# Kernel tuning notes

Measured on AMD Instinct MI355X. Metric: run time of the kernel, lower is better.

The kernel has to match this reference:

```python
import jax, jax.numpy as jnp
import numpy as np

H = 4        # num_heads
R = 5        # dilation_rate
W = 49       # window_size
D = 256      # d_model // 2
B = 32
N = 4900     # must be divisible by W*R = 245


def setup_inputs() -> dict:
    key = jax.random.key(0)
    k1, k2, k3, k4, k5 = jax.random.split(key, 5)
    s = 1.0 / np.sqrt(D)
    return {
        "emb": jax.random.normal(k1, (B, N, D), dtype=jnp.float32),
        "Wq": jax.random.normal(k2, (D, D), dtype=jnp.float32) * s,
        "bq": jax.random.normal(k3, (D,), dtype=jnp.float32) * s,
        "Wo": jax.random.normal(k4, (D, D), dtype=jnp.float32) * s,
        "bo": jax.random.normal(k5, (D,), dtype=jnp.float32) * s,
    }


def reference(emb, Wq, bq, Wo, bo):
    b, n, d = emb.shape
    dh = d // H
    g = n // (W * R)  # number of segments
    # Original forward uses q_proj for q, k AND v (faithful to source bug).
    q = emb @ Wq.T + bq  # [B, N, D]
    # Dilated local windows: token index = g*(W*R) + i*R + r.
    # Tokens sharing (segment g, dilation offset r) attend densely over i in [0, W).
    x = q.reshape(b, g, W, R, H, dh)
    scale = jnp.asarray(dh, q.dtype) ** -0.5
    scores = jnp.einsum("bgirhd,bgjrhd->bgrhij", x, x) * scale  # [B,G,R,H,W,W]
    attn = jax.nn.softmax(scores, axis=-1)
    out = jnp.einsum("bgrhij,bgjrhd->bgirhd", attn, x)  # [B,G,W,R,H,dh]
    out = out.reshape(b, n, d)
    return out @ Wo.T + bo
```

## Files before the change

kernel.cpp:

```cpp
#include <hip/hip_runtime.h>
#include <hip/hip_bf16.h>
#include <math.h>

#define NH     4
#define RD     5
#define WW     49
#define DM     256
#define BATCH  32
#define NTOK   4900
#define GSEG   20
#define SEG    245

typedef short bf16x8 __attribute__((ext_vector_type(8)));
typedef short bf16x4 __attribute__((ext_vector_type(4)));
typedef float f32x4  __attribute__((ext_vector_type(4)));

__device__ __forceinline__ short f2bf(float f) {
    union { __hip_bfloat16 h; short s; } u;
    u.h = __float2bfloat16(f);
    return u.s;
}

__device__ __forceinline__ int qix(int row, int col) {
    return row * 256 + (col ^ ((row & 7) << 3));
}
__device__ __forceinline__ int tix(int d, int j) {
    return 64 * 256 + d * 64 + (j ^ ((d & 7) << 3));
}

__global__ __launch_bounds__(256)
void wcvt(const float* __restrict__ Wq, const float* __restrict__ Wo,
          short* __restrict__ Wqb, short* __restrict__ Wob) {
    int t = blockIdx.x * 256 + threadIdx.x;
    const float* src = (t < 16384) ? Wq : Wo;
    short* dst = (t < 16384) ? Wqb : Wob;
    int i = (t & 16383) * 4;
    float4 v = *(const float4*)(src + i);
    bf16x4 o = { f2bf(v.x), f2bf(v.y), f2bf(v.z), f2bf(v.w) };
    *(bf16x4*)(dst + i) = o;
}

__global__ __launch_bounds__(256, 2)
void fused(const float* __restrict__ emb, const short* __restrict__ Wqb,
           const float* __restrict__ bq, const short* __restrict__ Wob,
           const float* __restrict__ bo, float* __restrict__ out) {
    __shared__ __align__(16) short sm[64 * 256 + 256 * 64];

    const int tid = threadIdx.x;
    const int wv = tid >> 6, ln = tid & 63, lc = ln & 15, lq = ln >> 4;

    const int bid = blockIdx.x;
    const int L = (bid & 7) * 400 + (bid >> 3);
    const int b = L / 100;
    const int rem = L - b * 100;
    const int g = rem / 5, r = rem - (rem / 5) * 5;
    const size_t tok0 = (size_t)b * NTOK + (size_t)g * SEG + r;
    const int n0 = wv * 64;

    {
        const float* ar[4];
        const short* br[4];
        #pragma unroll
        for (int mi = 0; mi < 4; mi++) {
            int t = mi * 16 + lc;
            t = (t > WW - 1) ? (WW - 1) : t;
            ar[mi] = emb + (tok0 + (size_t)t * RD) * DM + lq * 8;
        }
        #pragma unroll
        for (int ni = 0; ni < 4; ni++)
            br[ni] = Wqb + (size_t)(n0 + ni * 16 + lc) * DM + lq * 8;

        f32x4 acc[4][4] = {};
        for (int k0 = 0; k0 < DM; k0 += 32) {
            bf16x8 af[4], bfr[4];
            #pragma unroll
            for (int mi = 0; mi < 4; mi++) {
                float4 v0 = *(const float4*)(ar[mi] + k0);
                float4 v1 = *(const float4*)(ar[mi] + k0 + 4);
                bf16x8 t8 = { f2bf(v0.x), f2bf(v0.y), f2bf(v0.z), f2bf(v0.w),
                              f2bf(v1.x), f2bf(v1.y), f2bf(v1.z), f2bf(v1.w) };
                af[mi] = t8;
            }
            #pragma unroll
            for (int ni = 0; ni < 4; ni++) bfr[ni] = *(const bf16x8*)(br[ni] + k0);
            #pragma unroll
            for (int mi = 0; mi < 4; mi++)
                #pragma unroll
                for (int ni = 0; ni < 4; ni++)
                    acc[mi][ni] = __builtin_amdgcn_mfma_f32_16x16x32_bf16(
                        af[mi], bfr[ni], acc[mi][ni], 0, 0, 0);
        }
        float bv[4];
        #pragma unroll
        for (int ni = 0; ni < 4; ni++) bv[ni] = bq[n0 + ni * 16 + lc];
        #pragma unroll
        for (int mi = 0; mi < 4; mi++)
            #pragma unroll
            for (int rg = 0; rg < 4; rg++) {
                const int t = mi * 16 + lq * 4 + rg;
                #pragma unroll
                for (int ni = 0; ni < 4; ni++) {
                    const int col = n0 + ni * 16 + lc;
                    const short s = (t < WW) ? f2bf(acc[mi][ni][rg] + bv[ni])
                                             : (short)0;
                    sm[qix(t, col)] = s;
                    sm[tix(col, t)] = s;
                }
            }
    }
    __syncthreads();

    {
        const int c0 = n0;
        bf16x8 xa[4][2];
        #pragma unroll
        for (int mi = 0; mi < 4; mi++) {
            xa[mi][0] = *(const bf16x8*)&sm[qix(mi * 16 + lc, c0 + lq * 8)];
            xa[mi][1] = *(const bf16x8*)&sm[qix(mi * 16 + lc, c0 + 32 + lq * 8)];
        }
        f32x4 sa[4][4] = {};
        #pragma unroll
        for (int mi = 0; mi < 4; mi++)
            #pragma unroll
            for (int ni = 0; ni < 4; ni++) {
                sa[mi][ni] = __builtin_amdgcn_mfma_f32_16x16x32_bf16(
                    xa[mi][0], xa[ni][0], sa[mi][ni], 0, 0, 0);
                sa[mi][ni] = __builtin_amdgcn_mfma_f32_16x16x32_bf16(
                    xa[mi][1], xa[ni][1], sa[mi][ni], 0, 0, 0);
            }
        #pragma unroll
        for (int mi = 0; mi < 4; mi++)
            #pragma unroll
            for (int rg = 0; rg < 4; rg++) {
                float s[4];
                float m = -1e30f;
                #pragma unroll
                for (int ni = 0; ni < 4; ni++) {
                    s[ni] = sa[mi][ni][rg] * 0.125f;
                    if (ni * 16 + lc < WW) m = fmaxf(m, s[ni]);
                }
                m = fmaxf(m, __shfl_xor(m, 1));
                m = fmaxf(m, __shfl_xor(m, 2));
                m = fmaxf(m, __shfl_xor(m, 4));
                m = fmaxf(m, __shfl_xor(m, 8));
                float e4[4], l_ = 0.f;
                #pragma unroll
                for (int ni = 0; ni < 4; ni++) {
                    e4[ni] = (ni * 16 + lc < WW) ? __expf(s[ni] - m) : 0.f;
                    l_ += e4[ni];
                }
                l_ += __shfl_xor(l_, 1);
                l_ += __shfl_xor(l_, 2);
                l_ += __shfl_xor(l_, 4);
                l_ += __shfl_xor(l_, 8);
                const float inv = 1.f / l_;
                const int i = mi * 16 + lq * 4 + rg;
                #pragma unroll
                for (int ni = 0; ni < 4; ni++)
                    sm[qix(i, c0 + ni * 16 + lc)] = f2bf(e4[ni] * inv);
            }
        bf16x8 pa[4][2], pb[4][2];
        #pragma unroll
        for (int mi = 0; mi < 4; mi++) {
            pa[mi][0] = *(const bf16x8*)&sm[qix(mi * 16 + lc, c0 + lq * 8)];
            pa[mi][1] = *(const bf16x8*)&sm[qix(mi * 16 + lc, c0 + 32 + lq * 8)];
        }
        #pragma unroll
        for (int ni = 0; ni < 4; ni++) {
            pb[ni][0] = *(const bf16x8*)&sm[tix(c0 + ni * 16 + lc, lq * 8)];
            pb[ni][1] = *(const bf16x8*)&sm[tix(c0 + ni * 16 + lc, 32 + lq * 8)];
        }
        f32x4 oa[4][4] = {};
        #pragma unroll
        for (int mi = 0; mi < 4; mi++)
            #pragma unroll
            for (int ni = 0; ni < 4; ni++) {
                oa[mi][ni] = __builtin_amdgcn_mfma_f32_16x16x32_bf16(
                    pa[mi][0], pb[ni][0], oa[mi][ni], 0, 0, 0);
                oa[mi][ni] = __builtin_amdgcn_mfma_f32_16x16x32_bf16(
                    pa[mi][1], pb[ni][1], oa[mi][ni], 0, 0, 0);
            }
        #pragma unroll
        for (int mi = 0; mi < 4; mi++)
            #pragma unroll
            for (int rg = 0; rg < 4; rg++) {
                const int i = mi * 16 + lq * 4 + rg;
                if (i < WW) {
                    #pragma unroll
                    for (int ni = 0; ni < 4; ni++)
                        sm[qix(i, c0 + ni * 16 + lc)] = f2bf(oa[mi][ni][rg]);
                }
            }
    }
    __syncthreads();

    {
        const short* br[4];
        #pragma unroll
        for (int ni = 0; ni < 4; ni++)
            br[ni] = Wob + (size_t)(n0 + ni * 16 + lc) * DM + lq * 8;
        int trow[4];
        #pragma unroll
        for (int mi = 0; mi < 4; mi++) {
            int t = mi * 16 + lc;
            trow[mi] = (t > WW - 1) ? (WW - 1) : t;
        }
        f32x4 acc[4][4] = {};
        for (int k0 = 0; k0 < DM; k0 += 32) {
            bf16x8 af[4], bfr[4];
            #pragma unroll
            for (int mi = 0; mi < 4; mi++)
                af[mi] = *(const bf16x8*)&sm[qix(trow[mi], k0 + lq * 8)];
            #pragma unroll
            for (int ni = 0; ni < 4; ni++) bfr[ni] = *(const bf16x8*)(br[ni] + k0);
            #pragma unroll
            for (int mi = 0; mi < 4; mi++)
                #pragma unroll
                for (int ni = 0; ni < 4; ni++)
                    acc[mi][ni] = __builtin_amdgcn_mfma_f32_16x16x32_bf16(
                        af[mi], bfr[ni], acc[mi][ni], 0, 0, 0);
        }
        float bv[4];
        #pragma unroll
        for (int ni = 0; ni < 4; ni++) bv[ni] = bo[n0 + ni * 16 + lc];
        #pragma unroll
        for (int mi = 0; mi < 4; mi++)
            #pragma unroll
            for (int rg = 0; rg < 4; rg++) {
                const int t = mi * 16 + lq * 4 + rg;
                if (t < WW) {
                    float* op = out + (tok0 + (size_t)t * RD) * DM + n0;
                    #pragma unroll
                    for (int ni = 0; ni < 4; ni++)
                        op[ni * 16 + lc] = acc[mi][ni][rg] + bv[ni];
                }
            }
    }
}

extern "C" void kernel_launch(void* const* d_in, const int* in_sizes, int n_in,
                              void* d_out, int out_size, void* d_ws, size_t ws_size,
                              hipStream_t stream) {
    const float* emb = (const float*)d_in[0];
    const float* Wq  = (const float*)d_in[1];
    const float* bq  = (const float*)d_in[2];
    const float* Wo  = (const float*)d_in[3];
    const float* bo  = (const float*)d_in[4];
    float* out = (float*)d_out;

    short* Wqb = (short*)d_ws;
    short* Wob = Wqb + DM * DM;

    wcvt<<<dim3(128), dim3(256), 0, stream>>>(Wq, Wo, Wqb, Wob);
    fused<<<dim3(BATCH * GSEG * RD), dim3(256), 0, stream>>>(
        emb, Wqb, bq, Wob, bo, out);
}
```

Baseline: 473.1 us.

## Split window rows across 8 waves and software-pipeline global loads in GEMMs

Blocks grow from 256 to 512 threads: each of 8 waves now owns 32 token rows by 64 columns instead of 64 rows, which halves accumulator registers per wave and lets launch bounds ask for 4 blocks per CU. The Q and output projection loops are fully unrolled with register double-buffering, so the next k-slice of emb and weights loads while the current MFMAs run. The block-index swizzle across XCDs is removed. An extra barrier separates the score reads from the in-place probability writes, because waves now share rows. The risks are more barriers, duplicate loads of the B-side Q tiles, and possible register spills under the tighter bounds.

```diff
diff --git a/kernel.cpp b/kernel.cpp
--- a/kernel.cpp
+++ b/kernel.cpp
@@ -40,7 +40,7 @@
     *(bf16x4*)(dst + i) = o;
 }
 
-__global__ __launch_bounds__(256, 2)
+__global__ __launch_bounds__(512, 4)
 void fused(const float* __restrict__ emb, const short* __restrict__ Wqb,
            const float* __restrict__ bq, const short* __restrict__ Wob,
            const float* __restrict__ bo, float* __restrict__ out) {
@@ -50,57 +50,87 @@
     const int wv = tid >> 6, ln = tid & 63, lc = ln & 15, lq = ln >> 4;
 
     const int bid = blockIdx.x;
-    const int L = (bid & 7) * 400 + (bid >> 3);
-    const int b = L / 100;
-    const int rem = L - b * 100;
+    const int b = bid / 100;
+    const int rem = bid - b * 100;
     const int g = rem / 5, r = rem - (rem / 5) * 5;
     const size_t tok0 = (size_t)b * NTOK + (size_t)g * SEG + r;
-    const int n0 = wv * 64;
+
+    const int wn = (wv & 3) * 64;
+    const int wm = (wv >> 2) * 32;
 
     {
-        const float* ar[4];
+        const float* ar[2];
         const short* br[4];
         #pragma unroll
-        for (int mi = 0; mi < 4; mi++) {
-            int t = mi * 16 + lc;
+        for (int mi = 0; mi < 2; mi++) {
+            int t = wm + mi * 16 + lc;
             t = (t > WW - 1) ? (WW - 1) : t;
             ar[mi] = emb + (tok0 + (size_t)t * RD) * DM + lq * 8;
         }
         #pragma unroll
         for (int ni = 0; ni < 4; ni++)
-            br[ni] = Wqb + (size_t)(n0 + ni * 16 + lc) * DM + lq * 8;
-
-        f32x4 acc[4][4] = {};
-        for (int k0 = 0; k0 < DM; k0 += 32) {
-            bf16x8 af[4], bfr[4];
-            #pragma unroll
-            for (int mi = 0; mi < 4; mi++) {
-                float4 v0 = *(const float4*)(ar[mi] + k0);
-                float4 v1 = *(const float4*)(ar[mi] + k0 + 4);
-                bf16x8 t8 = { f2bf(v0.x), f2bf(v0.y), f2bf(v0.z), f2bf(v0.w),
-                              f2bf(v1.x), f2bf(v1.y), f2bf(v1.z), f2bf(v1.w) };
-                af[mi] = t8;
-            }
-            #pragma unroll
-            for (int ni = 0; ni < 4; ni++) bfr[ni] = *(const bf16x8*)(br[ni] + k0);
-            #pragma unroll
-            for (int mi = 0; mi < 4; mi++)
+            br[ni] = Wqb + (size_t)(wn + ni * 16 + lc) * DM + lq * 8;
+
+        f32x4 acc[2][4] = {};
+        float4 va[2][2];
+        bf16x8 wc[4];
+        #pragma unroll
+        for (int mi = 0; mi < 2; mi++) {
+            va[mi][0] = *(const float4*)(ar[mi]);
+            va[mi][1] = *(const float4*)(ar[mi] + 4);
+        }
+        #pragma unroll
+        for (int ni = 0; ni < 4; ni++) wc[ni] = *(const bf16x8*)(br[ni]);
+
+        #pragma unroll
+        for (int ks = 0; ks < 8; ks++) {
+            float4 vn[2][2];
+            bf16x8 wnx[4];
+            if (ks < 7) {
+                const int kn = ks * 32 + 32;
+                #pragma unroll
+                for (int mi = 0; mi < 2; mi++) {
+                    vn[mi][0] = *(const float4*)(ar[mi] + kn);
+                    vn[mi][1] = *(const float4*)(ar[mi] + kn + 4);
+                }
+                #pragma unroll
+                for (int ni = 0; ni < 4; ni++)
+                    wnx[ni] = *(const bf16x8*)(br[ni] + kn);
+            }
+            bf16x8 af[2];
+            #pragma unroll
+            for (int mi = 0; mi < 2; mi++) {
+                af[mi] = (bf16x8){ f2bf(va[mi][0].x), f2bf(va[mi][0].y),
+                                   f2bf(va[mi][0].z), f2bf(va[mi][0].w),
+                                   f2bf(va[mi][1].x), f2bf(va[mi][1].y),
+                                   f2bf(va[mi][1].z), f2bf(va[mi][1].w) };
+            }
+            #pragma unroll
+            for (int mi = 0; mi < 2; mi++)
                 #pragma unroll
                 for (int ni = 0; ni < 4; ni++)
                     acc[mi][ni] = __builtin_amdgcn_mfma_f32_16x16x32_bf16(
-                        af[mi], bfr[ni], acc[mi][ni], 0, 0, 0);
+                        af[mi], wc[ni], acc[mi][ni], 0, 0, 0);
+            if (ks < 7) {
+                #pragma unroll
+                for (int mi = 0; mi < 2; mi++) {
+                    va[mi][0] = vn[mi][0]; va[mi][1] = vn[mi][1];
+                }
+                #pragma unroll
+                for (int ni = 0; ni < 4; ni++) wc[ni] = wnx[ni];
+            }
         }
         float bv[4];
         #pragma unroll
-        for (int ni = 0; ni < 4; ni++) bv[ni] = bq[n0 + ni * 16 + lc];
-        #pragma unroll
-        for (int mi = 0; mi < 4; mi++)
+        for (int ni = 0; ni < 4; ni++) bv[ni] = bq[wn + ni * 16 + lc];
+        #pragma unroll
+        for (int mi = 0; mi < 2; mi++)
             #pragma unroll
             for (int rg = 0; rg < 4; rg++) {
-                const int t = mi * 16 + lq * 4 + rg;
+                const int t = wm + mi * 16 + lq * 4 + rg;
                 #pragma unroll
                 for (int ni = 0; ni < 4; ni++) {
-                    const int col = n0 + ni * 16 + lc;
+                    const int col = wn + ni * 16 + lc;
                     const short s = (t < WW) ? f2bf(acc[mi][ni][rg] + bv[ni])
                                              : (short)0;
                     sm[qix(t, col)] = s;
@@ -111,25 +141,32 @@
     __syncthreads();
 
     {
-        const int c0 = n0;
-        bf16x8 xa[4][2];
-        #pragma unroll
-        for (int mi = 0; mi < 4; mi++) {
-            xa[mi][0] = *(const bf16x8*)&sm[qix(mi * 16 + lc, c0 + lq * 8)];
-            xa[mi][1] = *(const bf16x8*)&sm[qix(mi * 16 + lc, c0 + 32 + lq * 8)];
-        }
-        f32x4 sa[4][4] = {};
-        #pragma unroll
-        for (int mi = 0; mi < 4; mi++)
+        const int c0 = wn, m0r = wm;
+        bf16x8 xa[2][2], xb[4][2];
+        #pragma unroll
+        for (int mi = 0; mi < 2; mi++) {
+            xa[mi][0] = *(const bf16x8*)&sm[qix(m0r + mi * 16 + lc, c0 + lq * 8)];
+            xa[mi][1] = *(const bf16x8*)&sm[qix(m0r + mi * 16 + lc, c0 + 32 + lq * 8)];
+        }
+        #pragma unroll
+        for (int ni = 0; ni < 4; ni++) {
+            xb[ni][0] = *(const bf16x8*)&sm[qix(ni * 16 + lc, c0 + lq * 8)];
+            xb[ni][1] = *(const bf16x8*)&sm[qix(ni * 16 + lc, c0 + 32 + lq * 8)];
+        }
+        f32x4 sa[2][4] = {};
+        #pragma unroll
+        for (int mi = 0; mi < 2; mi++)
             #pragma unroll
             for (int ni = 0; ni < 4; ni++) {
                 sa[mi][ni] = __builtin_amdgcn_mfma_f32_16x16x32_bf16(
-                    xa[mi][0], xa[ni][0], sa[mi][ni], 0, 0, 0);
+                    xa[mi][0], xb[ni][0], sa[mi][ni], 0, 0, 0);
                 sa[mi][ni] = __builtin_amdgcn_mfma_f32_16x16x32_bf16(
-                    xa[mi][1], xa[ni][1], sa[mi][ni], 0, 0, 0);
-            }
-        #pragma unroll
-        for (int mi = 0; mi < 4; mi++)
+                    xa[mi][1], xb[ni][1], sa[mi][ni], 0, 0, 0);
+            }
+        __syncthreads();
+
+        #pragma unroll
+        for (int mi = 0; mi < 2; mi++)
             #pragma unroll
             for (int rg = 0; rg < 4; rg++) {
                 float s[4];
@@ -154,25 +191,25 @@
                 l_ += __shfl_xor(l_, 4);
                 l_ += __shfl_xor(l_, 8);
                 const float inv = 1.f / l_;
-                const int i = mi * 16 + lq * 4 + rg;
-                #pragma unroll
-                for (int ni = 0; ni < 4; ni++)
-                    sm[qix(i, c0 + ni * 16 + lc)] = f2bf(e4[ni] * inv);
-            }
-        bf16x8 pa[4][2], pb[4][2];
-        #pragma unroll
-        for (int mi = 0; mi < 4; mi++) {
-            pa[mi][0] = *(const bf16x8*)&sm[qix(mi * 16 + lc, c0 + lq * 8)];
-            pa[mi][1] = *(const bf16x8*)&sm[qix(mi * 16 + lc, c0 + 32 + lq * 8)];
+                const int pr = m0r + mi * 16 + lq * 4 + rg;
+                #pragma unroll
+                for (int ni = 0; ni < 4; ni++)
+                    sm[qix(pr, c0 + ni * 16 + lc)] = f2bf(e4[ni] * inv);
+            }
+        bf16x8 pa[2][2], pb[4][2];
+        #pragma unroll
+        for (int mi = 0; mi < 2; mi++) {
+            pa[mi][0] = *(const bf16x8*)&sm[qix(m0r + mi * 16 + lc, c0 + lq * 8)];
+            pa[mi][1] = *(const bf16x8*)&sm[qix(m0r + mi * 16 + lc, c0 + 32 + lq * 8)];
         }
         #pragma unroll
         for (int ni = 0; ni < 4; ni++) {
             pb[ni][0] = *(const bf16x8*)&sm[tix(c0 + ni * 16 + lc, lq * 8)];
             pb[ni][1] = *(const bf16x8*)&sm[tix(c0 + ni * 16 + lc, 32 + lq * 8)];
         }
-        f32x4 oa[4][4] = {};
-        #pragma unroll
-        for (int mi = 0; mi < 4; mi++)
+        f32x4 oa[2][4] = {};
+        #pragma unroll
+        for (int mi = 0; mi < 2; mi++)
             #pragma unroll
             for (int ni = 0; ni < 4; ni++) {
                 oa[mi][ni] = __builtin_amdgcn_mfma_f32_16x16x32_bf16(
@@ -181,10 +218,10 @@
                     pa[mi][1], pb[ni][1], oa[mi][ni], 0, 0, 0);
             }
         #pragma unroll
-        for (int mi = 0; mi < 4; mi++)
+        for (int mi = 0; mi < 2; mi++)
             #pragma unroll
             for (int rg = 0; rg < 4; rg++) {
-                const int i = mi * 16 + lq * 4 + rg;
+                const int i = m0r + mi * 16 + lq * 4 + rg;
                 if (i < WW) {
                     #pragma unroll
                     for (int ni = 0; ni < 4; ni++)
@@ -198,38 +235,51 @@
         const short* br[4];
         #pragma unroll
         for (int ni = 0; ni < 4; ni++)
-            br[ni] = Wob + (size_t)(n0 + ni * 16 + lc) * DM + lq * 8;
-        int trow[4];
-        #pragma unroll
-        for (int mi = 0; mi < 4; mi++) {
-            int t = mi * 16 + lc;
+            br[ni] = Wob + (size_t)(wn + ni * 16 + lc) * DM + lq * 8;
+        int trow[2];
+        #pragma unroll
+        for (int mi = 0; mi < 2; mi++) {
+            int t = wm + mi * 16 + lc;
             trow[mi] = (t > WW - 1) ? (WW - 1) : t;
         }
-        f32x4 acc[4][4] = {};
-        for (int k0 = 0; k0 < DM; k0 += 32) {
-            bf16x8 af[4], bfr[4];
-            #pragma unroll
-            for (int mi = 0; mi < 4; mi++)
-                af[mi] = *(const bf16x8*)&sm[qix(trow[mi], k0 + lq * 8)];
-            #pragma unroll
-            for (int ni = 0; ni < 4; ni++) bfr[ni] = *(const bf16x8*)(br[ni] + k0);
-            #pragma unroll
-            for (int mi = 0; mi < 4; mi++)
+        f32x4 acc[2][4] = {};
+        bf16x8 wc[4];
+        #pragma unroll
+        for (int ni = 0; ni < 4; ni++) wc[ni] = *(const bf16x8*)(br[ni]);
+
+        #pragma unroll
+        for (int ks = 0; ks < 8; ks++) {
+            bf16x8 wnx[4];
+            if (ks < 7) {
+                #pragma unroll
+                for (int ni = 0; ni < 4; ni++)
+                    wnx[ni] = *(const bf16x8*)(br[ni] + ks * 32 + 32);
+            }
+            bf16x8 af[2];
+            #pragma unroll
+            for (int mi = 0; mi < 2; mi++)
+                af[mi] = *(const bf16x8*)&sm[qix(trow[mi], ks * 32 + lq * 8)];
+            #pragma unroll
+            for (int mi = 0; mi < 2; mi++)
                 #pragma unroll
                 for (int ni = 0; ni < 4; ni++)
                     acc[mi][ni] = __builtin_amdgcn_mfma_f32_16x16x32_bf16(
-                        af[mi], bfr[ni], acc[mi][ni], 0, 0, 0);
+                        af[mi], wc[ni], acc[mi][ni], 0, 0, 0);
+            if (ks < 7) {
+                #pragma unroll
+                for (int ni = 0; ni < 4; ni++) wc[ni] = wnx[ni];
+            }
         }
         float bv[4];
         #pragma unroll
-        for (int ni = 0; ni < 4; ni++) bv[ni] = bo[n0 + ni * 16 + lc];
-        #pragma unroll
-        for (int mi = 0; mi < 4; mi++)
+        for (int ni = 0; ni < 4; ni++) bv[ni] = bo[wn + ni * 16 + lc];
+        #pragma unroll
+        for (int mi = 0; mi < 2; mi++)
             #pragma unroll
             for (int rg = 0; rg < 4; rg++) {
-                const int t = mi * 16 + lq * 4 + rg;
+                const int t = wm + mi * 16 + lq * 4 + rg;
                 if (t < WW) {
-                    float* op = out + (tok0 + (size_t)t * RD) * DM + n0;
+                    float* op = out + (tok0 + (size_t)t * RD) * DM + wn;
                     #pragma unroll
                     for (int ni = 0; ni < 4; ni++)
                         op[ni * 16 + lc] = acc[mi][ni][rg] + bv[ni];
@@ -252,6 +302,6 @@
     short* Wob = Wqb + DM * DM;
 
     wcvt<<<dim3(128), dim3(256), 0, stream>>>(Wq, Wo, Wqb, Wob);
-    fused<<<dim3(BATCH * GSEG * RD), dim3(256), 0, stream>>>(
+    fused<<<dim3(BATCH * GSEG * RD), dim3(512), 0, stream>>>(
         emb, Wqb, bq, Wob, bo, out);
 }
```

New measurement: 504.6 us. 1.07x slower.

## Stage embedding tile into LDS via direct global-to-LDS loads and prefetch weights

Applied to the files above, without the earlier changes.

The fp32 embedding rows for each window are copied straight into shared memory with global_load_lds using an XOR-swizzled layout. Each row is fetched as a full coalesced 1 KB line, replacing the scattered 32-byte per-lane global reads of the Q projection. Both projection GEMMs are fully unrolled, and the weight fragments are double-buffered in registers so the next K-slice loads while the current MFMAs run. The XCD-aware block index remap is removed, and padded rows 49..63 of the staged tile are left uninitialised; they only feed outputs that get discarded.

```diff
diff --git a/kernel.cpp b/kernel.cpp
--- a/kernel.cpp
+++ b/kernel.cpp
@@ -19,6 +19,12 @@
     union { __hip_bfloat16 h; short s; } u;
     u.h = __float2bfloat16(f);
     return u.s;
+}
+
+__device__ __forceinline__ void gl_lds16(const void* g, void* l) {
+    __builtin_amdgcn_global_load_lds(
+        (const __attribute__((address_space(1))) void*)g,
+        (__attribute__((address_space(3))) void*)l, 16, 0, 0);
 }
 
 __device__ __forceinline__ int qix(int row, int col) {
@@ -44,55 +50,69 @@
 void fused(const float* __restrict__ emb, const short* __restrict__ Wqb,
            const float* __restrict__ bq, const short* __restrict__ Wob,
            const float* __restrict__ bo, float* __restrict__ out) {
-    __shared__ __align__(16) short sm[64 * 256 + 256 * 64];
+    __shared__ __align__(16) short sm[64 * 256 + 64 * 256];
+    float* As = (float*)sm;
 
     const int tid = threadIdx.x;
     const int wv = tid >> 6, ln = tid & 63, lc = ln & 15, lq = ln >> 4;
 
     const int bid = blockIdx.x;
-    const int L = (bid & 7) * 400 + (bid >> 3);
-    const int b = L / 100;
-    const int rem = L - b * 100;
+    const int b = bid / 100;
+    const int rem = bid - b * 100;
     const int g = rem / 5, r = rem - (rem / 5) * 5;
     const size_t tok0 = (size_t)b * NTOK + (size_t)g * SEG + r;
-    const int n0 = wv * 64;
-
-    {
-        const float* ar[4];
+    const int wn = wv * 64;
+
+    for (int p = wv; p < WW; p += 4)
+        gl_lds16(emb + (tok0 + (size_t)p * RD) * DM +
+                     (size_t)((ln ^ ((p & 7) << 1)) << 2),
+                 (char*)sm + p * 1024);
+    float bvq = bq[wn + lc];
+    __syncthreads();
+
+    f32x4 acc[4][4] = {};
+    {
         const short* br[4];
         #pragma unroll
-        for (int mi = 0; mi < 4; mi++) {
-            int t = mi * 16 + lc;
-            t = (t > WW - 1) ? (WW - 1) : t;
-            ar[mi] = emb + (tok0 + (size_t)t * RD) * DM + lq * 8;
-        }
-        #pragma unroll
         for (int ni = 0; ni < 4; ni++)
-            br[ni] = Wqb + (size_t)(n0 + ni * 16 + lc) * DM + lq * 8;
-
-        f32x4 acc[4][4] = {};
-        for (int k0 = 0; k0 < DM; k0 += 32) {
-            bf16x8 af[4], bfr[4];
+            br[ni] = Wqb + (size_t)(wn + ni * 16 + lc) * DM + lq * 8;
+        bf16x8 wb[2][4];
+        #pragma unroll
+        for (int ni = 0; ni < 4; ni++) wb[0][ni] = *(const bf16x8*)(br[ni]);
+        #pragma unroll
+        for (int ni = 0; ni < 4; ni++) wb[1][ni] = *(const bf16x8*)(br[ni] + 32);
+
+        #pragma unroll
+        for (int ks = 0; ks < 8; ks++) {
+            bf16x8 af[4];
             #pragma unroll
             for (int mi = 0; mi < 4; mi++) {
-                float4 v0 = *(const float4*)(ar[mi] + k0);
-                float4 v1 = *(const float4*)(ar[mi] + k0 + 4);
-                bf16x8 t8 = { f2bf(v0.x), f2bf(v0.y), f2bf(v0.z), f2bf(v0.w),
-                              f2bf(v1.x), f2bf(v1.y), f2bf(v1.z), f2bf(v1.w) };
-                af[mi] = t8;
-            }
-            #pragma unroll
-            for (int ni = 0; ni < 4; ni++) bfr[ni] = *(const bf16x8*)(br[ni] + k0);
+                const int t = mi * 16 + lc;
+                const int fo = t * 256 + (((ks * 8 + lq * 2) ^ ((t & 7) << 1)) << 2);
+                float4 lo = *(const float4*)&As[fo];
+                float4 hi = *(const float4*)&As[fo + 4];
+                af[mi] = (bf16x8){ f2bf(lo.x), f2bf(lo.y), f2bf(lo.z), f2bf(lo.w),
+                                   f2bf(hi.x), f2bf(hi.y), f2bf(hi.z), f2bf(hi.w) };
+            }
             #pragma unroll
             for (int mi = 0; mi < 4; mi++)
                 #pragma unroll
                 for (int ni = 0; ni < 4; ni++)
                     acc[mi][ni] = __builtin_amdgcn_mfma_f32_16x16x32_bf16(
-                        af[mi], bfr[ni], acc[mi][ni], 0, 0, 0);
-        }
+                        af[mi], wb[ks & 1][ni], acc[mi][ni], 0, 0, 0);
+            if (ks < 6) {
+                #pragma unroll
+                for (int ni = 0; ni < 4; ni++)
+                    wb[ks & 1][ni] = *(const bf16x8*)(br[ni] + (ks + 2) * 32);
+            }
+        }
+    }
+    __syncthreads();
+
+    {
         float bv[4];
         #pragma unroll
-        for (int ni = 0; ni < 4; ni++) bv[ni] = bq[n0 + ni * 16 + lc];
+        for (int ni = 0; ni < 4; ni++) bv[ni] = bq[wn + ni * 16 + lc];
         #pragma unroll
         for (int mi = 0; mi < 4; mi++)
             #pragma unroll
@@ -100,7 +120,7 @@
                 const int t = mi * 16 + lq * 4 + rg;
                 #pragma unroll
                 for (int ni = 0; ni < 4; ni++) {
-                    const int col = n0 + ni * 16 + lc;
+                    const int col = wn + ni * 16 + lc;
                     const short s = (t < WW) ? f2bf(acc[mi][ni][rg] + bv[ni])
                                              : (short)0;
                     sm[qix(t, col)] = s;
@@ -111,7 +131,7 @@
     __syncthreads();
 
     {
-        const int c0 = n0;
+        const int c0 = wn;
         bf16x8 xa[4][2];
         #pragma unroll
         for (int mi = 0; mi < 4; mi++) {
@@ -154,10 +174,10 @@
                 l_ += __shfl_xor(l_, 4);
                 l_ += __shfl_xor(l_, 8);
                 const float inv = 1.f / l_;
-                const int i = mi * 16 + lq * 4 + rg;
-                #pragma unroll
-                for (int ni = 0; ni < 4; ni++)
-                    sm[qix(i, c0 + ni * 16 + lc)] = f2bf(e4[ni] * inv);
+                const int pr = mi * 16 + lq * 4 + rg;
+                #pragma unroll
+                for (int ni = 0; ni < 4; ni++)
+                    sm[qix(pr, c0 + ni * 16 + lc)] = f2bf(e4[ni] * inv);
             }
         bf16x8 pa[4][2], pb[4][2];
         #pragma unroll
@@ -198,44 +218,55 @@
         const short* br[4];
         #pragma unroll
         for (int ni = 0; ni < 4; ni++)
-            br[ni] = Wob + (size_t)(n0 + ni * 16 + lc) * DM + lq * 8;
+            br[ni] = Wob + (size_t)(wn + ni * 16 + lc) * DM + lq * 8;
         int trow[4];
         #pragma unroll
         for (int mi = 0; mi < 4; mi++) {
             int t = mi * 16 + lc;
             trow[mi] = (t > WW - 1) ? (WW - 1) : t;
         }
-        f32x4 acc[4][4] = {};
-        for (int k0 = 0; k0 < DM; k0 += 32) {
-            bf16x8 af[4], bfr[4];
+        f32x4 ac3[4][4] = {};
+        bf16x8 wb[2][4];
+        #pragma unroll
+        for (int ni = 0; ni < 4; ni++) wb[0][ni] = *(const bf16x8*)(br[ni]);
+        #pragma unroll
+        for (int ni = 0; ni < 4; ni++) wb[1][ni] = *(const bf16x8*)(br[ni] + 32);
+
+        #pragma unroll
+        for (int ks = 0; ks < 8; ks++) {
+            bf16x8 af[4];
             #pragma unroll
             for (int mi = 0; mi < 4; mi++)
-                af[mi] = *(const bf16x8*)&sm[qix(trow[mi], k0 + lq * 8)];
-            #pragma unroll
-            for (int ni = 0; ni < 4; ni++) bfr[ni] = *(const bf16x8*)(br[ni] + k0);
+                af[mi] = *(const bf16x8*)&sm[qix(trow[mi], ks * 32 + lq * 8)];
             #pragma unroll
             for (int mi = 0; mi < 4; mi++)
                 #pragma unroll
                 for (int ni = 0; ni < 4; ni++)
-                    acc[mi][ni] = __builtin_amdgcn_mfma_f32_16x16x32_bf16(
-                        af[mi], bfr[ni], acc[mi][ni], 0, 0, 0);
+                    ac3[mi][ni] = __builtin_amdgcn_mfma_f32_16x16x32_bf16(
+                        af[mi], wb[ks & 1][ni], ac3[mi][ni], 0, 0, 0);
+            if (ks < 6) {
+                #pragma unroll
+                for (int ni = 0; ni < 4; ni++)
+                    wb[ks & 1][ni] = *(const bf16x8*)(br[ni] + (ks + 2) * 32);
+            }
         }
         float bv[4];
         #pragma unroll
-        for (int ni = 0; ni < 4; ni++) bv[ni] = bo[n0 + ni * 16 + lc];
+        for (int ni = 0; ni < 4; ni++) bv[ni] = bo[wn + ni * 16 + lc];
         #pragma unroll
         for (int mi = 0; mi < 4; mi++)
             #pragma unroll
             for (int rg = 0; rg < 4; rg++) {
                 const int t = mi * 16 + lq * 4 + rg;
                 if (t < WW) {
-                    float* op = out + (tok0 + (size_t)t * RD) * DM + n0;
+                    float* op = out + (tok0 + (size_t)t * RD) * DM + wn;
                     #pragma unroll
                     for (int ni = 0; ni < 4; ni++)
-                        op[ni * 16 + lc] = acc[mi][ni][rg] + bv[ni];
-                }
-            }
-    }
+                        op[ni * 16 + lc] = ac3[mi][ni][rg] + bv[ni];
+                }
+            }
+    }
+    (void)bvq;
 }
 
 extern "C" void kernel_launch(void* const* d_in, const int* in_sizes, int n_in,
```

Measured after the change: 421.7 us. 1.12x faster.
